# Kernel tuning notes

Hardware: AMD Instinct MI355X
Metric: run time of the kernel (lower is better)

## Reference

```python
import jax, jax.numpy as jnp
import numpy as np

N = 200_000   # nodes in batched graph
E = 400_000   # edges
D = 128       # embed_dim
L = 5         # num_layer
G = 1000      # number of graphs in batch
ATOM_V = 119  # atom vocab (OGB)
BOND_V = 5    # bond vocab (OGB)
OUT = 128     # output_dim
EPS = 1e-5


def setup_inputs() -> dict:
    key = jax.random.key(0)
    ks = jax.random.split(key, 16)
    inp = {
        "nfeat": jax.random.randint(ks[0], (N,), 0, ATOM_V),
        "efeat": jax.random.randint(ks[1], (E,), 0, BOND_V),
        "src": jax.random.randint(ks[2], (E,), 0, N),
        "dst": jax.random.randint(ks[3], (E,), 0, N),
        "node2graph": jnp.sort(jax.random.randint(ks[4], (N,), 0, G)),
        # learned parameters
        "atom_emb": jax.random.normal(ks[5], (ATOM_V, D), jnp.float32) * 0.02,
        "edge_emb": jax.random.normal(ks[6], (L, BOND_V, D), jnp.float32) * 0.02,
        "W": jax.random.normal(ks[7], (L, D, D), jnp.float32) * 0.02,
        "b": jnp.zeros((L, D), jnp.float32),
        "gamma": jnp.ones((L, D), jnp.float32),
        "beta": jnp.zeros((L, D), jnp.float32),
        "W1": jax.random.normal(ks[8], (D, D), jnp.float32) * 0.02,
        "b1": jnp.zeros((D,), jnp.float32),
        "W2": jax.random.normal(ks[9], (D, OUT), jnp.float32) * 0.02,
        "b2": jnp.zeros((OUT,), jnp.float32),
    }
    return inp


def reference(nfeat, efeat, src, dst, node2graph,
              atom_emb, edge_emb, W, b, gamma, beta, W1, b1, W2, b2):
    h = atom_emb[nfeat]                                  # [N, D]
    # in-degree + 1 (GCNConvLayer degree norm)
    deg = jax.ops.segment_sum(jnp.ones((E,), h.dtype), dst, num_segments=N) + 1.0
    for l in range(L):
        e = edge_emb[l][efeat]                           # [E, D] edge encoder
        m = h[src] + e                                   # u_add_e
        neigh = jax.ops.segment_sum(m, dst, num_segments=N)  # fn.sum -> 'neigh'
        h = ((h + neigh) / deg[:, None]) @ W[l] + b[l]   # project_node_feat
        # batch norm over nodes (training-mode batch stats), affine
        mu = jnp.mean(h, axis=0)
        var = jnp.var(h, axis=0)
        h = (h - mu) * jax.lax.rsqrt(var + EPS) * gamma[l] + beta[l]
        h = jax.nn.relu(h)                               # activation; dropout=eval
    # global mean pooling per graph
    cnt = jax.ops.segment_sum(jnp.ones((N,), h.dtype), node2graph, num_segments=G)
    g = jax.ops.segment_sum(h, node2graph, num_segments=G) / jnp.maximum(cnt, 1.0)[:, None]
    # predict MLP (dropout in eval mode = identity)
    out = jax.nn.relu(g @ W1 + b1) @ W2 + b2             # [G, OUT]
    return out
```

## Files before the change

### kernel.cpp

```cpp
#include <hip/hip_runtime.h>
#include <hip/hip_bf16.h>
#include <cstddef>

#define NN 200000
#define NE 400000
#define DD 128
#define NL 5
#define NG 1000
#define BOND_V 5
#define BM 32
#define NBLK (NN / BM)
#define MAXD 16
#define CHUNK 200
#define NB_SCAN 200
#define CH 1000
#define EPS 1e-5f
#define XS 136

typedef __bf16 bf16x8 __attribute__((ext_vector_type(8)));
typedef float floatx4 __attribute__((ext_vector_type(4)));

__device__ __forceinline__ unsigned short f2bf(float f) {
    unsigned int u = __float_as_uint(f);
    u = (u + 0x7fffu + ((u >> 16) & 1u)) >> 16;
    return (unsigned short)u;
}
__device__ __forceinline__ float bf2f(unsigned short s) {
    return __uint_as_float(((unsigned int)s) << 16);
}
__device__ __forceinline__ float4 bf4_to_f4(uint2 v) {
    float4 o;
    o.x = __uint_as_float(v.x << 16);
    o.y = __uint_as_float(v.x & 0xffff0000u);
    o.z = __uint_as_float(v.y << 16);
    o.w = __uint_as_float(v.y & 0xffff0000u);
    return o;
}

__global__ void k_setup1(const int* __restrict__ dst, int* __restrict__ cnt,
                         const int* __restrict__ n2g, float* __restrict__ gcnt,
                         const float* __restrict__ W, unsigned short* __restrict__ Wht,
                         unsigned short* __restrict__ Wlt) {
    int e = blockIdx.x * blockDim.x + threadIdx.x;
    if (e < NE) atomicAdd(&cnt[dst[e]], 1);
    if (e < NN) atomicAdd(&gcnt[n2g[e]], 1.0f);
    if (e < NL * DD * DD) {
        int l = e / (DD * DD), rem = e % (DD * DD);
        int k = rem / DD, n = rem % DD;
        float v = W[e];
        unsigned short hb = f2bf(v);
        unsigned short lb = f2bf(v - bf2f(hb));
        size_t o = (size_t)l * DD * DD + (size_t)n * DD + k;
        Wht[o] = hb; Wlt[o] = lb;
    }
}

__global__ void k_scan1(const int* __restrict__ cnt, int* __restrict__ bsum) {
    __shared__ int sh[256];
    int b = blockIdx.x, t = threadIdx.x;
    int s = 0;
    if (t < CH / 4) {
        int base = b * CH + t * 4;
        s = cnt[base] + cnt[base + 1] + cnt[base + 2] + cnt[base + 3];
    }
    sh[t] = s;
    __syncthreads();
    if (t == 0) {
        int tot = 0;
        for (int i = 0; i < CH / 4; i++) tot += sh[i];
        bsum[b] = tot;
    }
}

__global__ void k_scan2(const int* __restrict__ bsum, int* __restrict__ bpre,
                        int* __restrict__ off) {
    if (threadIdx.x == 0) {
        int run = 0;
        for (int i = 0; i < NB_SCAN; i++) { bpre[i] = run; run += bsum[i]; }
        off[NN] = NE;
    }
}

__global__ void k_scan3(const int* __restrict__ cnt, const int* __restrict__ bpre,
                        int* __restrict__ off, int* __restrict__ cur,
                        float* __restrict__ rdeg) {
    __shared__ int sh[256];
    int b = blockIdx.x, t = threadIdx.x;
    int base = b * CH + t * 4;
    int c0 = 0, c1 = 0, c2 = 0, c3 = 0, s = 0;
    if (t < CH / 4) {
        c0 = cnt[base]; c1 = cnt[base + 1]; c2 = cnt[base + 2]; c3 = cnt[base + 3];
        s = c0 + c1 + c2 + c3;
    }
    sh[t] = s;
    __syncthreads();
    if (t == 0) {
        int run = bpre[b];
        for (int i = 0; i < CH / 4; i++) { int v = sh[i]; sh[i] = run; run += v; }
    }
    __syncthreads();
    if (t < CH / 4) {
        int run = sh[t];
        off[base] = run; cur[base] = run; run += c0;
        off[base + 1] = run; cur[base + 1] = run; run += c1;
        off[base + 2] = run; cur[base + 2] = run; run += c2;
        off[base + 3] = run; cur[base + 3] = run;
        rdeg[base]     = 1.0f / (float)(c0 + 1);
        rdeg[base + 1] = 1.0f / (float)(c1 + 1);
        rdeg[base + 2] = 1.0f / (float)(c2 + 1);
        rdeg[base + 3] = 1.0f / (float)(c3 + 1);
    }
}

__global__ void k_bucket(const int* __restrict__ src, const int* __restrict__ dst,
                         const int* __restrict__ efeat, int* __restrict__ cur,
                         int* __restrict__ esrc, int* __restrict__ eft) {
    int e = blockIdx.x * blockDim.x + threadIdx.x;
    if (e < NE) {
        int p = atomicAdd(&cur[dst[e]], 1);
        esrc[p] = src[e];
        eft[p] = efeat[e];
    }
}

__global__ void k_pad(const int* __restrict__ off, const int* __restrict__ esrc,
                      const int* __restrict__ eft, int* __restrict__ pent,
                      int* __restrict__ bmaxd) {
    __shared__ int offL[BM + 1];
    __shared__ int mx;
    int b = blockIdx.x, tid = threadIdx.x;
    if (tid == 0) mx = 0;
    if (tid <= BM) offL[tid] = off[b * BM + tid];
    __syncthreads();
    if (tid < BM) atomicMax(&mx, offL[tid + 1] - offL[tid]);
    __syncthreads();
    int maxd = mx;
    if (tid == 0) bmaxd[b] = maxd;
    int jmax = maxd < MAXD ? maxd : MAXD;
    int tot = jmax * BM;
    int* pb = pent + (size_t)b * MAXD * BM;
    for (int idx = tid; idx < tot; idx += 256) {
        int j = idx >> 5, r = idx & 31;
        int d = offL[r + 1] - offL[r];
        int v;
        if (j < d) { int e = offL[r] + j; v = esrc[e] | (eft[e] << 18); }
        else v = (5 << 18);
        pb[idx] = v;
    }
}

__device__ __forceinline__ float4 bnrelu4(float4 x, float4 m, float4 r, float4 g, float4 b) {
    float4 o;
    o.x = fmaxf(0.f, (x.x - m.x) * r.x * g.x + b.x);
    o.y = fmaxf(0.f, (x.y - m.y) * r.y * g.y + b.y);
    o.z = fmaxf(0.f, (x.z - m.z) * r.z * g.z + b.z);
    o.w = fmaxf(0.f, (x.w - m.w) * r.w * g.w + b.w);
    return o;
}

__global__ __launch_bounds__(256)
void k_fused(const void* __restrict__ basep, const int* __restrict__ nfeat, int first,
             const int* __restrict__ off, const int* __restrict__ esrc,
             const int* __restrict__ eft, const int* __restrict__ pent,
             const int* __restrict__ bmaxd, const float* __restrict__ eemb,
             const float* __restrict__ rdeg,
             const float* __restrict__ muP, const float* __restrict__ rsP,
             const float* __restrict__ gamma, const float* __restrict__ beta,
             const unsigned short* __restrict__ Wht, const unsigned short* __restrict__ Wlt,
             const float* __restrict__ bias,
             unsigned short* __restrict__ C, float* __restrict__ part) {
    __shared__ unsigned short Xh[BM * XS];
    __shared__ unsigned short Xl[BM * XS];
    __shared__ float eS[6 * DD];
    __shared__ float red[4 * DD];
    __shared__ int offL[BM + 1];

    const float* baseF = (const float*)basep;
    const unsigned short* baseB = (const unsigned short*)basep;

    int tid = threadIdx.x;
    int n0 = blockIdx.x * BM;
    if (tid < 160) *(float4*)(eS + tid * 4) = *(const float4*)(eemb + tid * 4);
    else if (tid < 192) *(float4*)(eS + tid * 4) = (float4){0.f, 0.f, 0.f, 0.f};
    if (tid <= BM) offL[tid] = off[n0 + tid];

    int lane32 = tid & 31, grp = tid >> 5;
    int c4 = lane32 << 2;
    float4 m4, r4, g4, b4;
    if (!first) {
        m4 = *(const float4*)(muP + c4);
        r4 = *(const float4*)(rsP + c4);
        g4 = *(const float4*)(gamma + c4);
        b4 = *(const float4*)(beta + c4);
    }
    __syncthreads();

    float4 acc[4];
    #pragma unroll
    for (int i = 0; i < 4; i++) {
        int n = n0 + grp * 4 + i;
        float4 a;
        if (first) {
            a = *(const float4*)(baseF + (size_t)nfeat[n] * DD + c4);
        } else {
            uint2 g = *(const uint2*)(baseB + (size_t)n * DD + c4);
            a = bnrelu4(bf4_to_f4(g), m4, r4, g4, b4);
        }
        acc[i] = a;
    }

    int maxd = bmaxd[blockIdx.x];
    int jmax = maxd < MAXD ? maxd : MAXD;
    const int* pb = pent + (size_t)blockIdx.x * MAXD * BM + grp * 4;
    for (int j = 0; j < jmax; j++) {
        int v0 = pb[j * BM + 0];
        int v1 = pb[j * BM + 1];
        int v2 = pb[j * BM + 2];
        int v3 = pb[j * BM + 3];
        int s0 = v0 & 0x3FFFF, f0 = v0 >> 18;
        int s1 = v1 & 0x3FFFF, f1 = v1 >> 18;
        int s2 = v2 & 0x3FFFF, f2 = v2 >> 18;
        int s3 = v3 & 0x3FFFF, f3 = v3 >> 18;
        float4 h0, h1, h2, h3;
        if (first) {
            h0 = *(const float4*)(baseF + (size_t)nfeat[s0] * DD + c4);
            h1 = *(const float4*)(baseF + (size_t)nfeat[s1] * DD + c4);
            h2 = *(const float4*)(baseF + (size_t)nfeat[s2] * DD + c4);
            h3 = *(const float4*)(baseF + (size_t)nfeat[s3] * DD + c4);
        } else {
            uint2 g0 = *(const uint2*)(baseB + (size_t)s0 * DD + c4);
            uint2 g1 = *(const uint2*)(baseB + (size_t)s1 * DD + c4);
            uint2 g2 = *(const uint2*)(baseB + (size_t)s2 * DD + c4);
            uint2 g3 = *(const uint2*)(baseB + (size_t)s3 * DD + c4);
            h0 = bnrelu4(bf4_to_f4(g0), m4, r4, g4, b4);
            h1 = bnrelu4(bf4_to_f4(g1), m4, r4, g4, b4);
            h2 = bnrelu4(bf4_to_f4(g2), m4, r4, g4, b4);
            h3 = bnrelu4(bf4_to_f4(g3), m4, r4, g4, b4);
        }
        float w0 = (f0 == 5) ? 0.f : 1.f;
        float w1 = (f1 == 5) ? 0.f : 1.f;
        float w2 = (f2 == 5) ? 0.f : 1.f;
        float w3 = (f3 == 5) ? 0.f : 1.f;
        float4 e0 = *(const float4*)(eS + f0 * DD + c4);
        float4 e1 = *(const float4*)(eS + f1 * DD + c4);
        float4 e2 = *(const float4*)(eS + f2 * DD + c4);
        float4 e3 = *(const float4*)(eS + f3 * DD + c4);
        acc[0].x += (h0.x + e0.x) * w0; acc[0].y += (h0.y + e0.y) * w0;
        acc[0].z += (h0.z + e0.z) * w0; acc[0].w += (h0.w + e0.w) * w0;
        acc[1].x += (h1.x + e1.x) * w1; acc[1].y += (h1.y + e1.y) * w1;
        acc[1].z += (h1.z + e1.z) * w1; acc[1].w += (h1.w + e1.w) * w1;
        acc[2].x += (h2.x + e2.x) * w2; acc[2].y += (h2.y + e2.y) * w2;
        acc[2].z += (h2.z + e2.z) * w2; acc[2].w += (h2.w + e2.w) * w2;
        acc[3].x += (h3.x + e3.x) * w3; acc[3].y += (h3.y + e3.y) * w3;
        acc[3].z += (h3.z + e3.z) * w3; acc[3].w += (h3.w + e3.w) * w3;
    }

    if (maxd > MAXD) {
        #pragma unroll
        for (int i = 0; i < 4; i++) {
            int r = grp * 4 + i;
            for (int e = offL[r] + MAXD; e < offL[r + 1]; e++) {
                int s = esrc[e], f = eft[e];
                float4 hv;
                if (first) {
                    hv = *(const float4*)(baseF + (size_t)nfeat[s] * DD + c4);
                } else {
                    uint2 g = *(const uint2*)(baseB + (size_t)s * DD + c4);
                    hv = bnrelu4(bf4_to_f4(g), m4, r4, g4, b4);
                }
                const float* ep = eS + f * DD + c4;
                acc[i].x += hv.x + ep[0]; acc[i].y += hv.y + ep[1];
                acc[i].z += hv.z + ep[2]; acc[i].w += hv.w + ep[3];
            }
        }
    }

    #pragma unroll
    for (int i = 0; i < 4; i++) {
        int r = grp * 4 + i;
        float rd = rdeg[n0 + r];
        float ax = acc[i].x * rd, ay = acc[i].y * rd, az = acc[i].z * rd, aw = acc[i].w * rd;
        unsigned short h0 = f2bf(ax), h1 = f2bf(ay), h2 = f2bf(az), h3 = f2bf(aw);
        unsigned short l0 = f2bf(ax - bf2f(h0));
        unsigned short l1 = f2bf(ay - bf2f(h1));
        unsigned short l2 = f2bf(az - bf2f(h2));
        unsigned short l3 = f2bf(aw - bf2f(h3));
        uint2 hv2, lv2;
        hv2.x = (unsigned)h0 | ((unsigned)h1 << 16);
        hv2.y = (unsigned)h2 | ((unsigned)h3 << 16);
        lv2.x = (unsigned)l0 | ((unsigned)l1 << 16);
        lv2.y = (unsigned)l2 | ((unsigned)l3 << 16);
        *(uint2*)(Xh + r * XS + c4) = hv2;
        *(uint2*)(Xl + r * XS + c4) = lv2;
    }
    __syncthreads();

    int lane = tid & 63, w = tid >> 6;
    int m16 = lane & 15, quad = lane >> 4;
    int rowTile = w & 1;
    int colBase = (w >> 1) << 6;
    int rowA = rowTile * 16 + m16;

    floatx4 acc4[4];
    #pragma unroll
    for (int t = 0; t < 4; t++) acc4[t] = (floatx4){0.f, 0.f, 0.f, 0.f};

    #pragma unroll
    for (int kp = 0; kp < 4; kp++) {
        bf16x8 ah = *(const bf16x8*)(Xh + rowA * XS + kp * 32 + quad * 8);
        bf16x8 al = *(const bf16x8*)(Xl + rowA * XS + kp * 32 + quad * 8);
        #pragma unroll
        for (int t = 0; t < 4; t++) {
            int ncol = colBase + t * 16 + m16;
            bf16x8 bh = *(const bf16x8*)(Wht + (size_t)ncol * DD + kp * 32 + quad * 8);
            bf16x8 bl = *(const bf16x8*)(Wlt + (size_t)ncol * DD + kp * 32 + quad * 8);
            acc4[t] = __builtin_amdgcn_mfma_f32_16x16x32_bf16(ah, bh, acc4[t], 0, 0, 0);
            acc4[t] = __builtin_amdgcn_mfma_f32_16x16x32_bf16(ah, bl, acc4[t], 0, 0, 0);
            acc4[t] = __builtin_amdgcn_mfma_f32_16x16x32_bf16(al, bh, acc4[t], 0, 0, 0);
        }
    }
    __syncthreads();

    float* redS = red;
    float* redQ = red + 2 * DD;
    unsigned short* Cs = Xh;
    #pragma unroll
    for (int t = 0; t < 4; t++) {
        int col = colBase + t * 16 + m16;
        float bv = bias[col];
        float s = 0.f, q = 0.f;
        #pragma unroll
        for (int rr = 0; rr < 4; rr++) {
            float vv = acc4[t][rr] + bv;
            s += vv; q += vv * vv;
            Cs[(rowTile * 16 + quad * 4 + rr) * XS + col] = f2bf(vv);
        }
        s += __shfl_xor(s, 16); q += __shfl_xor(q, 16);
        s += __shfl_xor(s, 32); q += __shfl_xor(q, 32);
        if (lane < 16) { redS[rowTile * DD + col] = s; redQ[rowTile * DD + col] = q; }
    }
    __syncthreads();

    #pragma unroll
    for (int it = 0; it < 2; it++) {
        int idx = it * 256 + tid;
        int row = idx >> 4, q16 = idx & 15;
        uint4 v = *(const uint4*)(Cs + row * XS + q16 * 8);
        *(uint4*)(C + (size_t)(n0 + row) * DD + q16 * 8) = v;
    }
    if (tid < DD) {
        float ss = redS[tid] + redS[DD + tid];
        float qq = redQ[tid] + redQ[DD + tid];
        part[(size_t)tid * NBLK + blockIdx.x] = ss;
        part[(size_t)(DD + tid) * NBLK + blockIdx.x] = qq;
    }
}

__global__ void k_stats(const float* __restrict__ part,
                        float* __restrict__ mu, float* __restrict__ rsig) {
    int col = blockIdx.x;
    float s = 0.f, q = 0.f;
    for (int i = threadIdx.x; i < NBLK; i += 256) {
        s += part[(size_t)col * NBLK + i];
        q += part[(size_t)(DD + col) * NBLK + i];
    }
    #pragma unroll
    for (int o = 32; o > 0; o >>= 1) {
        s += __shfl_down(s, o);
        q += __shfl_down(q, o);
    }
    __shared__ float sh[8];
    int lane = threadIdx.x & 63, w = threadIdx.x >> 6;
    if (lane == 0) { sh[w] = s; sh[4 + w] = q; }
    __syncthreads();
    if (threadIdx.x == 0) {
        float S = sh[0] + sh[1] + sh[2] + sh[3];
        float Q = sh[4] + sh[5] + sh[6] + sh[7];
        float m = S / (float)NN;
        float v = Q / (float)NN - m * m;
        mu[col] = m;
        rsig[col] = rsqrtf(v + EPS);
    }
}

__global__ void k_bnpool(const unsigned short* __restrict__ A, const int* __restrict__ n2g,
                         const float* __restrict__ mu, const float* __restrict__ rsig,
                         const float* __restrict__ gamma, const float* __restrict__ beta,
                         float* __restrict__ gsum) {
    int j = threadIdx.x;
    int n0 = blockIdx.x * CHUNK;
    float m = mu[j], r = rsig[j], ga = gamma[j], be = beta[j];
    int cur = n2g[n0];
    float acc = 0.f;
    for (int i = 0; i < CHUNK; i++) {
        int n = n0 + i;
        int gg = n2g[n];
        if (gg != cur) {
            atomicAdd(&gsum[(size_t)cur * DD + j], acc);
            acc = 0.f;
            cur = gg;
        }
        float x = bf2f(A[(size_t)n * DD + j]);
        x = fmaxf(0.f, (x - m) * r * ga + be);
        acc += x;
    }
    atomicAdd(&gsum[(size_t)cur * DD + j], acc);
}

__global__ void k_mlp(const float* __restrict__ gsum, const float* __restrict__ gcnt,
                      const float* __restrict__ W1, const float* __restrict__ b1,
                      const float* __restrict__ W2, const float* __restrict__ b2,
                      float* __restrict__ out) {
    __shared__ float gs[DD], hs[DD];
    int gid = blockIdx.x, j = threadIdx.x;
    float inv = 1.0f / fmaxf(gcnt[gid], 1.0f);
    gs[j] = gsum[(size_t)gid * DD + j] * inv;
    __syncthreads();
    float a = b1[j];
    for (int k = 0; k < DD; k++) a += gs[k] * W1[k * DD + j];
    hs[j] = fmaxf(a, 0.f);
    __syncthreads();
    float o = b2[j];
    for (int k = 0; k < DD; k++) o += hs[k] * W2[k * DD + j];
    out[(size_t)gid * DD + j] = o;
}

extern "C" void kernel_launch(void* const* d_in, const int* in_sizes, int n_in,
                              void* d_out, int out_size, void* d_ws, size_t ws_size,
                              hipStream_t stream) {
    const int*   nfeat = (const int*)d_in[0];
    const int*   efeat = (const int*)d_in[1];
    const int*   src   = (const int*)d_in[2];
    const int*   dst   = (const int*)d_in[3];
    const int*   n2g   = (const int*)d_in[4];
    const float* aemb  = (const float*)d_in[5];
    const float* eemb  = (const float*)d_in[6];
    const float* Wl    = (const float*)d_in[7];
    const float* bl    = (const float*)d_in[8];
    const float* gam   = (const float*)d_in[9];
    const float* bet   = (const float*)d_in[10];
    const float* W1    = (const float*)d_in[11];
    const float* b1    = (const float*)d_in[12];
    const float* W2    = (const float*)d_in[13];
    const float* b2    = (const float*)d_in[14];
    float* out = (float*)d_out;

    unsigned short* H0 = (unsigned short*)d_ws;
    unsigned short* H1 = H0 + (size_t)NN * DD;
    float* rdeg = (float*)(H1 + (size_t)NN * DD);
    float* gsum = rdeg + NN;
    float* gcnt = gsum + (size_t)NG * DD;
    float* mu   = gcnt + NG;
    float* rsg  = mu + DD;
    float* part = rsg + DD;
    unsigned short* Wht = (unsigned short*)(part + (size_t)2 * DD * NBLK);
    unsigned short* Wlt = Wht + (size_t)NL * DD * DD;
    int* off   = (int*)(Wlt + (size_t)NL * DD * DD);
    int* cur   = off + NN + 1;
    int* esrc  = cur + NN;
    int* eft   = esrc + NE;
    int* cnt   = eft + NE;
    int* bsum  = cnt + NN;
    int* bpre  = bsum + NB_SCAN;
    int* bmaxd = bpre + NB_SCAN;
    int* pent  = bmaxd + NBLK;

    hipMemsetAsync(gsum, 0, (size_t)(NG * DD + NG) * sizeof(float), stream);
    hipMemsetAsync(cnt, 0, (size_t)NN * sizeof(int), stream);

    k_setup1<<<(NE + 255) / 256, 256, 0, stream>>>(dst, cnt, n2g, gcnt, Wl, Wht, Wlt);
    k_scan1<<<NB_SCAN, 256, 0, stream>>>(cnt, bsum);
    k_scan2<<<1, 64, 0, stream>>>(bsum, bpre, off);
    k_scan3<<<NB_SCAN, 256, 0, stream>>>(cnt, bpre, off, cur, rdeg);
    k_bucket<<<(NE + 255) / 256, 256, 0, stream>>>(src, dst, efeat, cur, esrc, eft);
    k_pad<<<NBLK, 256, 0, stream>>>(off, esrc, eft, pent, bmaxd);

    unsigned short* hcur = H0;
    for (int l = 0; l < NL; l++) {
        const void* base = (l == 0) ? (const void*)aemb : (const void*)hcur;
        unsigned short* hnext = (l == 0) ? H0 : ((hcur == H0) ? H1 : H0);
        const float* g_prev = (l == 0) ? gam : gam + (size_t)(l - 1) * DD;
        const float* b_prev = (l == 0) ? bet : bet + (size_t)(l - 1) * DD;
        k_fused<<<NBLK, 256, 0, stream>>>(base, nfeat, (l == 0) ? 1 : 0,
                                          off, esrc, eft, pent, bmaxd,
                                          eemb + (size_t)l * BOND_V * DD, rdeg,
                                          mu, rsg, g_prev, b_prev,
                                          Wht + (size_t)l * DD * DD,
                                          Wlt + (size_t)l * DD * DD,
                                          bl + (size_t)l * DD, hnext, part);
        k_stats<<<DD, 256, 0, stream>>>(part, mu, rsg);
        hcur = hnext;
    }
    k_bnpool<<<NN / CHUNK, DD, 0, stream>>>(hcur, n2g, mu, rsg,
                                            gam + (size_t)(NL - 1) * DD,
                                            bet + (size_t)(NL - 1) * DD, gsum);
    k_mlp<<<NG, DD, 0, stream>>>(gsum, gcnt, W1, b1, W2, b2, out);
}
```

Measured before the change: 1.113 ms.

## Sort rows by degree within blocks and restructure batch-norm stats reduction

k_pad now sorts the 32 rows of each node block by in-degree and records a per-warp-group maximum degree plus a row permutation. k_fused processes rows in that permuted order, so each group of 4 rows loops only to its own max degree rather than the block max, cutting padded gather iterations. The stats reduction is also reorganised: partial sums are stored row-major per block, reduced by 125 blocks with atomics into a per-layer buffer, then finalised by a tiny kernel. This adds an extra kernel launch per layer and uses float atomics, which makes the summation order nondeterministic.

```diff
diff --git a/kernel.cpp b/kernel.cpp
--- a/kernel.cpp
+++ b/kernel.cpp
@@ -14,6 +14,7 @@
 #define CHUNK 200
 #define NB_SCAN 200
 #define CH 1000
+#define SB 125
 #define EPS 1e-5f
 #define XS 136
 
@@ -125,27 +126,42 @@
 
 __global__ void k_pad(const int* __restrict__ off, const int* __restrict__ esrc,
                       const int* __restrict__ eft, int* __restrict__ pent,
-                      int* __restrict__ bmaxd) {
+                      int* __restrict__ bperm, int* __restrict__ gmax) {
     __shared__ int offL[BM + 1];
-    __shared__ int mx;
+    __shared__ int degS[BM];
+    __shared__ int sortIdx[BM];
+    __shared__ int gmaxS[8];
     int b = blockIdx.x, tid = threadIdx.x;
-    if (tid == 0) mx = 0;
     if (tid <= BM) offL[tid] = off[b * BM + tid];
     __syncthreads();
-    if (tid < BM) atomicMax(&mx, offL[tid + 1] - offL[tid]);
-    __syncthreads();
-    int maxd = mx;
-    if (tid == 0) bmaxd[b] = maxd;
-    int jmax = maxd < MAXD ? maxd : MAXD;
-    int tot = jmax * BM;
-    int* pb = pent + (size_t)b * MAXD * BM;
-    for (int idx = tid; idx < tot; idx += 256) {
-        int j = idx >> 5, r = idx & 31;
-        int d = offL[r + 1] - offL[r];
-        int v;
-        if (j < d) { int e = offL[r] + j; v = esrc[e] | (eft[e] << 18); }
-        else v = (5 << 18);
-        pb[idx] = v;
+    if (tid < BM) degS[tid] = offL[tid + 1] - offL[tid];
+    __syncthreads();
+    if (tid < BM) {
+        int d = degS[tid], rank = 0;
+        #pragma unroll
+        for (int j = 0; j < BM; j++)
+            rank += (degS[j] > d) || (degS[j] == d && j < tid);
+        sortIdx[rank] = tid;
+    }
+    __syncthreads();
+    if (tid < 8) {
+        int g = degS[sortIdx[tid * 4]];
+        gmaxS[tid] = g;
+        gmax[b * 8 + tid] = g;
+    }
+    if (tid < BM) bperm[b * BM + tid] = sortIdx[tid];
+    __syncthreads();
+    for (int idx = tid; idx < BM * MAXD; idx += 256) {
+        int p = idx & 31, j = idx >> 5, g = p >> 2;
+        int gm = gmaxS[g]; if (gm > MAXD) gm = MAXD;
+        if (j < gm) {
+            int row = sortIdx[p];
+            int d = degS[row];
+            int v;
+            if (j < d) { int e = offL[row] + j; v = esrc[e] | (eft[e] << 18); }
+            else v = (5 << 18);
+            pent[(size_t)b * MAXD * BM + j * BM + p] = v;
+        }
     }
 }
 
@@ -162,8 +178,8 @@
 void k_fused(const void* __restrict__ basep, const int* __restrict__ nfeat, int first,
              const int* __restrict__ off, const int* __restrict__ esrc,
              const int* __restrict__ eft, const int* __restrict__ pent,
-             const int* __restrict__ bmaxd, const float* __restrict__ eemb,
-             const float* __restrict__ rdeg,
+             const int* __restrict__ bperm, const int* __restrict__ gmax,
+             const float* __restrict__ eemb, const float* __restrict__ rdeg,
              const float* __restrict__ muP, const float* __restrict__ rsP,
              const float* __restrict__ gamma, const float* __restrict__ beta,
              const unsigned short* __restrict__ Wht, const unsigned short* __restrict__ Wlt,
@@ -174,6 +190,8 @@
     __shared__ float eS[6 * DD];
     __shared__ float red[4 * DD];
     __shared__ int offL[BM + 1];
+    __shared__ int permL[BM];
+    __shared__ int gmL[8];
 
     const float* baseF = (const float*)basep;
     const unsigned short* baseB = (const unsigned short*)basep;
@@ -183,6 +201,8 @@
     if (tid < 160) *(float4*)(eS + tid * 4) = *(const float4*)(eemb + tid * 4);
     else if (tid < 192) *(float4*)(eS + tid * 4) = (float4){0.f, 0.f, 0.f, 0.f};
     if (tid <= BM) offL[tid] = off[n0 + tid];
+    if (tid < BM) permL[tid] = bperm[blockIdx.x * BM + tid];
+    if (tid < 8) gmL[tid] = gmax[blockIdx.x * 8 + tid];
 
     int lane32 = tid & 31, grp = tid >> 5;
     int c4 = lane32 << 2;
@@ -195,10 +215,14 @@
     }
     __syncthreads();
 
+    int rows[4];
+    #pragma unroll
+    for (int i = 0; i < 4; i++) rows[i] = permL[grp * 4 + i];
+
     float4 acc[4];
     #pragma unroll
     for (int i = 0; i < 4; i++) {
-        int n = n0 + grp * 4 + i;
+        int n = n0 + rows[i];
         float4 a;
         if (first) {
             a = *(const float4*)(baseF + (size_t)nfeat[n] * DD + c4);
@@ -209,8 +233,8 @@
         acc[i] = a;
     }
 
-    int maxd = bmaxd[blockIdx.x];
-    int jmax = maxd < MAXD ? maxd : MAXD;
+    int gmx = gmL[grp];
+    int jmax = gmx < MAXD ? gmx : MAXD;
     const int* pb = pent + (size_t)blockIdx.x * MAXD * BM + grp * 4;
     for (int j = 0; j < jmax; j++) {
         int v0 = pb[j * BM + 0];
@@ -255,11 +279,11 @@
         acc[3].z += (h3.z + e3.z) * w3; acc[3].w += (h3.w + e3.w) * w3;
     }
 
-    if (maxd > MAXD) {
+    if (gmx > MAXD) {
         #pragma unroll
         for (int i = 0; i < 4; i++) {
-            int r = grp * 4 + i;
-            for (int e = offL[r] + MAXD; e < offL[r + 1]; e++) {
+            int row = rows[i];
+            for (int e = offL[row] + MAXD; e < offL[row + 1]; e++) {
                 int s = esrc[e], f = eft[e];
                 float4 hv;
                 if (first) {
@@ -277,7 +301,7 @@
 
     #pragma unroll
     for (int i = 0; i < 4; i++) {
-        int r = grp * 4 + i;
+        int r = rows[i];
         float rd = rdeg[n0 + r];
         float ax = acc[i].x * rd, ay = acc[i].y * rd, az = acc[i].z * rd, aw = acc[i].w * rd;
         unsigned short h0 = f2bf(ax), h1 = f2bf(ay), h2 = f2bf(az), h3 = f2bf(aw);
@@ -351,36 +375,28 @@
     if (tid < DD) {
         float ss = redS[tid] + redS[DD + tid];
         float qq = redQ[tid] + redQ[DD + tid];
-        part[(size_t)tid * NBLK + blockIdx.x] = ss;
-        part[(size_t)(DD + tid) * NBLK + blockIdx.x] = qq;
-    }
-}
-
-__global__ void k_stats(const float* __restrict__ part,
-                        float* __restrict__ mu, float* __restrict__ rsig) {
-    int col = blockIdx.x;
-    float s = 0.f, q = 0.f;
-    for (int i = threadIdx.x; i < NBLK; i += 256) {
-        s += part[(size_t)col * NBLK + i];
-        q += part[(size_t)(DD + col) * NBLK + i];
-    }
-    #pragma unroll
-    for (int o = 32; o > 0; o >>= 1) {
-        s += __shfl_down(s, o);
-        q += __shfl_down(q, o);
-    }
-    __shared__ float sh[8];
-    int lane = threadIdx.x & 63, w = threadIdx.x >> 6;
-    if (lane == 0) { sh[w] = s; sh[4 + w] = q; }
-    __syncthreads();
-    if (threadIdx.x == 0) {
-        float S = sh[0] + sh[1] + sh[2] + sh[3];
-        float Q = sh[4] + sh[5] + sh[6] + sh[7];
-        float m = S / (float)NN;
-        float v = Q / (float)NN - m * m;
-        mu[col] = m;
-        rsig[col] = rsqrtf(v + EPS);
-    }
+        part[(size_t)blockIdx.x * 256 + tid] = ss;
+        part[(size_t)blockIdx.x * 256 + DD + tid] = qq;
+    }
+}
+
+__global__ void k_stats(const float* __restrict__ part, float* __restrict__ musum) {
+    int t = threadIdx.x;
+    float s = 0.f;
+    int base = blockIdx.x * (NBLK / SB);
+    for (int i = 0; i < NBLK / SB; i++)
+        s += part[(size_t)(base + i) * 256 + t];
+    atomicAdd(&musum[t], s);
+}
+
+__global__ void k_fin(const float* __restrict__ musum,
+                      float* __restrict__ mu, float* __restrict__ rsig) {
+    int t = threadIdx.x;
+    float S = musum[t], Q = musum[DD + t];
+    float m = S / (float)NN;
+    float v = Q / (float)NN - m * m;
+    mu[t] = m;
+    rsig[t] = rsqrtf(v + EPS);
 }
 
 __global__ void k_bnpool(const unsigned short* __restrict__ A, const int* __restrict__ n2g,
@@ -447,13 +463,14 @@
 
     unsigned short* H0 = (unsigned short*)d_ws;
     unsigned short* H1 = H0 + (size_t)NN * DD;
-    float* rdeg = (float*)(H1 + (size_t)NN * DD);
-    float* gsum = rdeg + NN;
-    float* gcnt = gsum + (size_t)NG * DD;
-    float* mu   = gcnt + NG;
-    float* rsg  = mu + DD;
-    float* part = rsg + DD;
-    unsigned short* Wht = (unsigned short*)(part + (size_t)2 * DD * NBLK);
+    float* rdeg  = (float*)(H1 + (size_t)NN * DD);
+    float* gsum  = rdeg + NN;
+    float* gcnt  = gsum + (size_t)NG * DD;
+    float* mu    = gcnt + NG;
+    float* rsg   = mu + DD;
+    float* musum = rsg + DD;
+    float* part  = musum + NL * 256;
+    unsigned short* Wht = (unsigned short*)(part + (size_t)NBLK * 256);
     unsigned short* Wlt = Wht + (size_t)NL * DD * DD;
     int* off   = (int*)(Wlt + (size_t)NL * DD * DD);
     int* cur   = off + NN + 1;
@@ -462,10 +479,12 @@
     int* cnt   = eft + NE;
     int* bsum  = cnt + NN;
     int* bpre  = bsum + NB_SCAN;
-    int* bmaxd = bpre + NB_SCAN;
-    int* pent  = bmaxd + NBLK;
-
-    hipMemsetAsync(gsum, 0, (size_t)(NG * DD + NG) * sizeof(float), stream);
+    int* bperm = bpre + NB_SCAN;
+    int* gmax  = bperm + (size_t)NBLK * BM;
+    int* pent  = gmax + (size_t)NBLK * 8;
+
+    hipMemsetAsync(gsum, 0,
+                   (size_t)(NG * DD + NG + 2 * DD + NL * 256) * sizeof(float), stream);
     hipMemsetAsync(cnt, 0, (size_t)NN * sizeof(int), stream);
 
     k_setup1<<<(NE + 255) / 256, 256, 0, stream>>>(dst, cnt, n2g, gcnt, Wl, Wht, Wlt);
@@ -473,7 +492,7 @@
     k_scan2<<<1, 64, 0, stream>>>(bsum, bpre, off);
     k_scan3<<<NB_SCAN, 256, 0, stream>>>(cnt, bpre, off, cur, rdeg);
     k_bucket<<<(NE + 255) / 256, 256, 0, stream>>>(src, dst, efeat, cur, esrc, eft);
-    k_pad<<<NBLK, 256, 0, stream>>>(off, esrc, eft, pent, bmaxd);
+    k_pad<<<NBLK, 256, 0, stream>>>(off, esrc, eft, pent, bperm, gmax);
 
     unsigned short* hcur = H0;
     for (int l = 0; l < NL; l++) {
@@ -482,13 +501,14 @@
         const float* g_prev = (l == 0) ? gam : gam + (size_t)(l - 1) * DD;
         const float* b_prev = (l == 0) ? bet : bet + (size_t)(l - 1) * DD;
         k_fused<<<NBLK, 256, 0, stream>>>(base, nfeat, (l == 0) ? 1 : 0,
-                                          off, esrc, eft, pent, bmaxd,
+                                          off, esrc, eft, pent, bperm, gmax,
                                           eemb + (size_t)l * BOND_V * DD, rdeg,
                                           mu, rsg, g_prev, b_prev,
                                           Wht + (size_t)l * DD * DD,
                                           Wlt + (size_t)l * DD * DD,
                                           bl + (size_t)l * DD, hnext, part);
-        k_stats<<<DD, 256, 0, stream>>>(part, mu, rsg);
+        k_stats<<<SB, 256, 0, stream>>>(part, musum + l * 256);
+        k_fin<<<1, DD, 0, stream>>>(musum + l * 256, mu, rsg);
         hcur = hnext;
     }
     k_bnpool<<<NN / CHUNK, DD, 0, stream>>>(hcur, n2g, mu, rsg,
```

Result: faster. 1.090 ms (-2.1%).
